# Optimization experiments

Measured on AMD Instinct MI355X. Metric: run time of the kernel, lower is better.

## Reference

```python
import jax, jax.numpy as jnp
import numpy as np

EPS = 1e-05
IN_FEATURES = 1024
OUT_FEATURES = 512
M = 65536


def setup_inputs() -> dict:
    key = jax.random.key(0)
    k_x, k_w, k_b = jax.random.split(key, 3)
    x = jax.random.normal(k_x, (M, IN_FEATURES), dtype=jnp.float32)
    # kaiming_uniform(a=sqrt(5)) on [out, in]: bound = sqrt(6/((1+a^2)*fan_in)) = 1/sqrt(fan_in)
    bound = 1.0 / np.sqrt(IN_FEATURES)
    weight = jax.random.uniform(k_w, (OUT_FEATURES, IN_FEATURES), dtype=jnp.float32,
                                minval=-bound, maxval=bound)
    bias = jax.random.uniform(k_b, (OUT_FEATURES,), dtype=jnp.float32,
                              minval=-bound, maxval=bound)
    gamma = jnp.ones((OUT_FEATURES,), dtype=jnp.float32)
    beta = jnp.zeros((OUT_FEATURES,), dtype=jnp.float32)
    scale = jnp.ones((1,), dtype=jnp.float32)
    return {"x": x, "weight": weight, "bias": bias,
            "gamma": gamma, "beta": beta, "scale": scale}


def reference(x, weight, bias, gamma, beta, scale):
    # GEMM + bias: [M, N]
    acc = jnp.einsum('mk,nk->mn', x, weight) + bias[None, :]
    # Row-wise normalization over N (as the fused kernel computes per row)
    mean = jnp.mean(acc, axis=1, keepdims=True)
    var = jnp.mean((acc - mean) ** 2, axis=1, keepdims=True)
    normalized = (acc - mean) / jnp.sqrt(var + EPS)
    scaled = (normalized * gamma[None, :] + beta[None, :]) * scale[0]
    # Row softmax over N
    return jax.nn.softmax(scaled, axis=1)
```

## Files before the change

### kernel.cpp

```cpp
#include <hip/hip_runtime.h>
#include <hip/hip_bf16.h>

constexpr int KD = 1024;
constexpr int ND = 512;
constexpr int NT = 32;
constexpr float EPSV = 1e-5f;

using f32x4  = __attribute__((ext_vector_type(4))) float;
using bf16x8 = __attribute__((ext_vector_type(8))) short;
using u16x8  = __attribute__((ext_vector_type(8))) unsigned short;

__device__ __forceinline__ unsigned short f2bf(float f) {
  unsigned int u = __builtin_bit_cast(unsigned int, f);
  return (unsigned short)((u + 0x7fffu + ((u >> 16) & 1u)) >> 16);
}

__device__ __forceinline__ u16x8 pack8(float4 a, float4 b) {
  u16x8 v;
  v[0] = f2bf(a.x); v[1] = f2bf(a.y); v[2] = f2bf(a.z); v[3] = f2bf(a.w);
  v[4] = f2bf(b.x); v[5] = f2bf(b.y); v[6] = f2bf(b.z); v[7] = f2bf(b.w);
  return v;
}

__device__ __forceinline__ unsigned short cvt1(float f) {
  __hip_bfloat16 h = __float2bfloat16(f);
  return __builtin_bit_cast(unsigned short, h);
}

#define SCHEDB()  __builtin_amdgcn_sched_barrier(0)

__global__ void wconvert_kernel(const float* __restrict__ w,
                                unsigned short* __restrict__ wb) {
  int uid = blockIdx.x * blockDim.x + threadIdx.x;
  int s   = uid >> 11;
  int nf  = (uid >> 6) & 31;
  int l   = uid & 63;
  int n   = nf * 16 + (l & 15);
  int k0  = s * 32 + (l >> 4) * 8;
  const float* src = w + n * KD + k0;
  float4 a = *reinterpret_cast<const float4*>(src);
  float4 b = *reinterpret_cast<const float4*>(src + 4);
  *reinterpret_cast<u16x8*>(wb + (size_t)uid * 8) = pack8(a, b);
}

__global__ __launch_bounds__(512, 4)
void fused_kernel(const float* __restrict__ x,
                  const unsigned short* __restrict__ wb,
                  const float* __restrict__ bias,
                  const float* __restrict__ gamma,
                  const float* __restrict__ beta,
                  const float* __restrict__ scalep,
                  float* __restrict__ out) {
  __shared__ unsigned short As[4][64 * 32];

  const int tid  = threadIdx.x;
  const int lane = tid & 63;
  const int wid  = tid >> 6;
  const int l15  = lane & 15;
  const int lg   = lane >> 4;

  const long bm  = (long)blockIdx.x * 64;

  f32x4 acc[4][4] = {};

  const int arow = tid >> 3;
  const int akq  = tid & 7;
  const float* asrc = x + (bm + arow) * KD + akq * 4;
  const int awb = arow * 64 + (((akq >> 1) ^ ((arow >> 1) & 3)) * 16)
                + ((akq & 1) * 8);

  const int swa = (lg ^ ((l15 >> 1) & 3)) * 16;
  int ard[4];
  #pragma unroll
  for (int mi = 0; mi < 4; ++mi) ard[mi] = (mi * 16 + l15) * 64 + swa;

  const unsigned short* bbase = wb + ((size_t)(wid * 4) * 64 + lane) * 8;

#define LOADA(t) (*reinterpret_cast<const float4*>(asrc + (t) * 32))

#define LOADB(t, r0, r1, r2, r3) do { \
    const unsigned short* bp_ = bbase + (size_t)(t) * 16384; \
    r0 = *reinterpret_cast<const bf16x8*>(bp_ + 0 * 512); \
    r1 = *reinterpret_cast<const bf16x8*>(bp_ + 1 * 512); \
    r2 = *reinterpret_cast<const bf16x8*>(bp_ + 2 * 512); \
    r3 = *reinterpret_cast<const bf16x8*>(bp_ + 3 * 512); } while (0)

#define WRITE_A(q_, bufi) do { \
    union { unsigned short s[4]; unsigned long long v; } c_; \
    c_.s[0] = cvt1(q_.x); c_.s[1] = cvt1(q_.y); \
    c_.s[2] = cvt1(q_.z); c_.s[3] = cvt1(q_.w); \
    *reinterpret_cast<unsigned long long*>((char*)As[bufi] + awb) = c_.v; } while (0)

#define COMPUTE(bufi, B0, B1, B2, B3) do { \
    const char* ab_ = (const char*)As[bufi]; \
    bf16x8 a0_ = *reinterpret_cast<const bf16x8*>(ab_ + ard[0]); \
    bf16x8 a1_ = *reinterpret_cast<const bf16x8*>(ab_ + ard[1]); \
    bf16x8 a2_ = *reinterpret_cast<const bf16x8*>(ab_ + ard[2]); \
    bf16x8 a3_ = *reinterpret_cast<const bf16x8*>(ab_ + ard[3]); \
    acc[0][0] = __builtin_amdgcn_mfma_f32_16x16x32_bf16(a0_, B0, acc[0][0], 0, 0, 0); \
    acc[0][1] = __builtin_amdgcn_mfma_f32_16x16x32_bf16(a0_, B1, acc[0][1], 0, 0, 0); \
    acc[0][2] = __builtin_amdgcn_mfma_f32_16x16x32_bf16(a0_, B2, acc[0][2], 0, 0, 0); \
    acc[0][3] = __builtin_amdgcn_mfma_f32_16x16x32_bf16(a0_, B3, acc[0][3], 0, 0, 0); \
    acc[1][0] = __builtin_amdgcn_mfma_f32_16x16x32_bf16(a1_, B0, acc[1][0], 0, 0, 0); \
    acc[1][1] = __builtin_amdgcn_mfma_f32_16x16x32_bf16(a1_, B1, acc[1][1], 0, 0, 0); \
    acc[1][2] = __builtin_amdgcn_mfma_f32_16x16x32_bf16(a1_, B2, acc[1][2], 0, 0, 0); \
    acc[1][3] = __builtin_amdgcn_mfma_f32_16x16x32_bf16(a1_, B3, acc[1][3], 0, 0, 0); \
    acc[2][0] = __builtin_amdgcn_mfma_f32_16x16x32_bf16(a2_, B0, acc[2][0], 0, 0, 0); \
    acc[2][1] = __builtin_amdgcn_mfma_f32_16x16x32_bf16(a2_, B1, acc[2][1], 0, 0, 0); \
    acc[2][2] = __builtin_amdgcn_mfma_f32_16x16x32_bf16(a2_, B2, acc[2][2], 0, 0, 0); \
    acc[2][3] = __builtin_amdgcn_mfma_f32_16x16x32_bf16(a2_, B3, acc[2][3], 0, 0, 0); \
    acc[3][0] = __builtin_amdgcn_mfma_f32_16x16x32_bf16(a3_, B0, acc[3][0], 0, 0, 0); \
    acc[3][1] = __builtin_amdgcn_mfma_f32_16x16x32_bf16(a3_, B1, acc[3][1], 0, 0, 0); \
    acc[3][2] = __builtin_amdgcn_mfma_f32_16x16x32_bf16(a3_, B2, acc[3][2], 0, 0, 0); \
    acc[3][3] = __builtin_amdgcn_mfma_f32_16x16x32_bf16(a3_, B3, acc[3][3], 0, 0, 0); \
    } while (0)

  float4 qaE, qaO;
  bf16x8 bc0, bc1, bc2, bc3, bn0, bn1, bn2, bn3;

  qaE = LOADA(0);
  qaO = LOADA(1);
  LOADB(0, bc0, bc1, bc2, bc3);
  WRITE_A(qaE, 0);
  WRITE_A(qaO, 1);
  __syncthreads();

  for (int t = 0; t < NT; t += 2) {
    const int b0 = t & 3;
    const int tp2 = (t + 2 < NT) ? t + 2 : NT - 1;
    const int tp3 = (t + 3 < NT) ? t + 3 : NT - 1;
    qaE = LOADA(tp2);
    qaO = LOADA(tp3);
    LOADB(t + 1 < NT ? t + 1 : NT - 1, bn0, bn1, bn2, bn3);
    SCHEDB();
    COMPUTE(b0, bc0, bc1, bc2, bc3);
    WRITE_A(qaE, (b0 + 2) & 3);
    LOADB(tp2, bc0, bc1, bc2, bc3);
    SCHEDB();
    COMPUTE((b0 + 1) & 3, bn0, bn1, bn2, bn3);
    WRITE_A(qaO, (b0 + 3) & 3);
    __syncthreads();
  }

  float* redS = (float*)As[0];
  float* redQ = redS + 576;
  float* rowA = redS + 1152;
  float* rowB = redS + 1216;

  const int col0 = wid * 64 + l15;
  const float sc = scalep[0];
  float bs4[4], gs4[4], bb4[4];
  #pragma unroll
  for (int ni = 0; ni < 4; ++ni) {
    bs4[ni] = bias[col0 + ni * 16];
    gs4[ni] = gamma[col0 + ni * 16] * sc;
    bb4[ni] = beta[col0 + ni * 16] * sc;
  }

  #pragma unroll
  for (int mi = 0; mi < 4; ++mi) {
    #pragma unroll
    for (int j = 0; j < 4; ++j) {
      float s = 0.f, q = 0.f;
      #pragma unroll
      for (int ni = 0; ni < 4; ++ni) {
        float v = acc[mi][ni][j] + bs4[ni];
        acc[mi][ni][j] = v;
        s += v;
        q = fmaf(v, v, q);
      }
      #pragma unroll
      for (int m = 1; m < 16; m <<= 1) {
        s += __shfl_xor(s, m, 64);
        q += __shfl_xor(q, m, 64);
      }
      if (l15 == 0) {
        int r = mi * 16 + lg * 4 + j;
        redS[r * 9 + wid] = s;
        redQ[r * 9 + wid] = q;
      }
    }
  }
  __syncthreads();
  if (tid < 64) {
    float s = 0.f, q = 0.f;
    #pragma unroll
    for (int k = 0; k < 8; ++k) { s += redS[tid * 9 + k]; q += redQ[tid * 9 + k]; }
    float mu = s * (1.f / ND);
    rowA[tid] = mu;
    rowB[tid] = rsqrtf(q * (1.f / ND) - mu * mu + EPSV);
  }
  __syncthreads();

  #pragma unroll
  for (int mi = 0; mi < 4; ++mi) {
    #pragma unroll
    for (int j = 0; j < 4; ++j) {
      int r = mi * 16 + lg * 4 + j;
      float mu = rowA[r], rs = rowB[r];
      float ps = 0.f;
      #pragma unroll
      for (int ni = 0; ni < 4; ++ni) {
        float v = (acc[mi][ni][j] - mu) * rs;
        v = fmaf(v, gs4[ni], bb4[ni]);
        float e = __expf(v);
        acc[mi][ni][j] = e;
        ps += e;
      }
      #pragma unroll
      for (int m = 1; m < 16; m <<= 1) ps += __shfl_xor(ps, m, 64);
      if (l15 == 0) redQ[r * 9 + wid] = ps;
    }
  }
  __syncthreads();
  if (tid < 64) {
    float s = 0.f;
    #pragma unroll
    for (int k = 0; k < 8; ++k) s += redQ[tid * 9 + k];
    rowB[tid] = 1.f / s;
  }
  __syncthreads();

  #pragma unroll
  for (int mi = 0; mi < 4; ++mi) {
    #pragma unroll
    for (int j = 0; j < 4; ++j) {
      int r = mi * 16 + lg * 4 + j;
      float rd = rowB[r];
      float* op = out + (bm + r) * ND + col0;
      #pragma unroll
      for (int ni = 0; ni < 4; ++ni)
        __builtin_nontemporal_store(acc[mi][ni][j] * rd, op + ni * 16);
    }
  }
#undef LOADA
#undef LOADB
#undef WRITE_A
#undef COMPUTE
}

__global__ void fused_fallback(const float* __restrict__ x,
                               const float* __restrict__ wf,
                               const float* __restrict__ bias,
                               const float* __restrict__ gamma,
                               const float* __restrict__ beta,
                               const float* __restrict__ scalep,
                               float* __restrict__ out) {
  long row = blockIdx.x;
  int t = threadIdx.x;
  float s = 0.f;
  const float* xr = x + row * KD;
  const float* wr_ = wf + (size_t)t * KD;
  for (int k = 0; k < KD; ++k) s += xr[k] * wr_[k];
  s += bias[t];
  __shared__ float buf[ND];
  buf[t] = s;
  __syncthreads();
  __shared__ float red[2];
  if (t == 0) {
    float sum = 0.f, sq = 0.f;
    for (int i = 0; i < ND; ++i) { sum += buf[i]; sq += buf[i] * buf[i]; }
    float mu = sum / ND;
    red[0] = mu;
    red[1] = rsqrtf(sq / ND - mu * mu + EPSV);
  }
  __syncthreads();
  float zv = (s - red[0]) * red[1] * gamma[t] * scalep[0] + beta[t] * scalep[0];
  buf[t] = zv;
  __syncthreads();
  __shared__ float red2[2];
  if (t == 0) {
    float mxv = -3.4e38f;
    for (int i = 0; i < ND; ++i) mxv = fmaxf(mxv, buf[i]);
    float den = 0.f;
    for (int i = 0; i < ND; ++i) den += __expf(buf[i] - mxv);
    red2[0] = mxv; red2[1] = 1.f / den;
  }
  __syncthreads();
  out[row * ND + t] = __expf(zv - red2[0]) * red2[1];
}

extern "C" void kernel_launch(void* const* d_in, const int* in_sizes, int n_in,
                              void* d_out, int out_size, void* d_ws, size_t ws_size,
                              hipStream_t stream) {
  const float* x     = (const float*)d_in[0];
  const float* w     = (const float*)d_in[1];
  const float* bias  = (const float*)d_in[2];
  const float* gamma = (const float*)d_in[3];
  const float* beta  = (const float*)d_in[4];
  const float* scale = (const float*)d_in[5];
  float* out = (float*)d_out;

  const int Mrows = in_sizes[0] / KD;
  const size_t wb_bytes = (size_t)ND * KD * sizeof(unsigned short);

  if (ws_size >= wb_bytes) {
    unsigned short* wbuf = (unsigned short*)d_ws;
    wconvert_kernel<<<(ND * KD / 8) / 256, 256, 0, stream>>>(w, wbuf);
    fused_kernel<<<Mrows / 64, 512, 0, stream>>>(x, wbuf, bias, gamma, beta,
                                                 scale, out);
  } else {
    fused_fallback<<<Mrows, ND, 0, stream>>>(x, w, bias, gamma, beta, scale, out);
  }
}
```

Before: 121.4 us.

## Give each wave a private double-buffered A tile to drop block barriers

Each of the eight waves now loads and converts the whole 64x32 fp32 A tile for every k-step into its own double-buffered LDS region. This removes the per-iteration __syncthreads from the main loop. The cost is that x is loaded and converted to bf16 eight times per block instead of once, which adds much more global/L2 traffic and VALU conversion work. LDS use per block also grows fourfold, which can lower how many blocks fit on a CU.

```diff
diff --git a/kernel.cpp b/kernel.cpp
--- a/kernel.cpp
+++ b/kernel.cpp
@@ -51,7 +51,7 @@
                   const float* __restrict__ beta,
                   const float* __restrict__ scalep,
                   float* __restrict__ out) {
-  __shared__ unsigned short As[4][64 * 32];
+  __shared__ unsigned short As[8][2][2048];
 
   const int tid  = threadIdx.x;
   const int lane = tid & 63;
@@ -63,86 +63,93 @@
 
   f32x4 acc[4][4] = {};
 
-  const int arow = tid >> 3;
-  const int akq  = tid & 7;
+  const int arow = lane >> 3;
+  const int akq  = lane & 7;
   const float* asrc = x + (bm + arow) * KD + akq * 4;
-  const int awb = arow * 64 + (((akq >> 1) ^ ((arow >> 1) & 3)) * 16)
-                + ((akq & 1) * 8);
-
-  const int swa = (lg ^ ((l15 >> 1) & 3)) * 16;
-  int ard[4];
-  #pragma unroll
-  for (int mi = 0; mi < 4; ++mi) ard[mi] = (mi * 16 + l15) * 64 + swa;
+  const int awb0 = arow * 64 + (((akq >> 1) ^ ((arow >> 1) & 3)) * 16)
+                 + ((akq & 1) * 8);
+
+  const int ardb = l15 * 64 + (lg ^ ((l15 >> 1) & 3)) * 16;
 
   const unsigned short* bbase = wb + ((size_t)(wid * 4) * 64 + lane) * 8;
 
-#define LOADA(t) (*reinterpret_cast<const float4*>(asrc + (t) * 32))
-
-#define LOADB(t, r0, r1, r2, r3) do { \
+  char* const buf0 = (char*)As[wid][0];
+  char* const buf1 = (char*)As[wid][1];
+
+#define ISSUE_A4(t, roff) do { \
+    qa0 = *reinterpret_cast<const float4*>(asrc + ((roff) + 0)  * KD + (t) * 32); \
+    qa1 = *reinterpret_cast<const float4*>(asrc + ((roff) + 8)  * KD + (t) * 32); \
+    qa2 = *reinterpret_cast<const float4*>(asrc + ((roff) + 16) * KD + (t) * 32); \
+    qa3 = *reinterpret_cast<const float4*>(asrc + ((roff) + 24) * KD + (t) * 32); } while (0)
+
+#define WRITE_A4(bufp, boff) do { \
+    union { unsigned short s[4]; unsigned long long v; } c0_, c1_, c2_, c3_; \
+    c0_.s[0] = cvt1(qa0.x); c0_.s[1] = cvt1(qa0.y); \
+    c0_.s[2] = cvt1(qa0.z); c0_.s[3] = cvt1(qa0.w); \
+    c1_.s[0] = cvt1(qa1.x); c1_.s[1] = cvt1(qa1.y); \
+    c1_.s[2] = cvt1(qa1.z); c1_.s[3] = cvt1(qa1.w); \
+    c2_.s[0] = cvt1(qa2.x); c2_.s[1] = cvt1(qa2.y); \
+    c2_.s[2] = cvt1(qa2.z); c2_.s[3] = cvt1(qa2.w); \
+    c3_.s[0] = cvt1(qa3.x); c3_.s[1] = cvt1(qa3.y); \
+    c3_.s[2] = cvt1(qa3.z); c3_.s[3] = cvt1(qa3.w); \
+    *reinterpret_cast<unsigned long long*>((bufp) + awb0 + (boff) + 0 * 512) = c0_.v; \
+    *reinterpret_cast<unsigned long long*>((bufp) + awb0 + (boff) + 1 * 512) = c1_.v; \
+    *reinterpret_cast<unsigned long long*>((bufp) + awb0 + (boff) + 2 * 512) = c2_.v; \
+    *reinterpret_cast<unsigned long long*>((bufp) + awb0 + (boff) + 3 * 512) = c3_.v; } while (0)
+
+#define ISSUE_B(t) do { \
     const unsigned short* bp_ = bbase + (size_t)(t) * 16384; \
-    r0 = *reinterpret_cast<const bf16x8*>(bp_ + 0 * 512); \
-    r1 = *reinterpret_cast<const bf16x8*>(bp_ + 1 * 512); \
-    r2 = *reinterpret_cast<const bf16x8*>(bp_ + 2 * 512); \
-    r3 = *reinterpret_cast<const bf16x8*>(bp_ + 3 * 512); } while (0)
-
-#define WRITE_A(q_, bufi) do { \
-    union { unsigned short s[4]; unsigned long long v; } c_; \
-    c_.s[0] = cvt1(q_.x); c_.s[1] = cvt1(q_.y); \
-    c_.s[2] = cvt1(q_.z); c_.s[3] = cvt1(q_.w); \
-    *reinterpret_cast<unsigned long long*>((char*)As[bufi] + awb) = c_.v; } while (0)
-
-#define COMPUTE(bufi, B0, B1, B2, B3) do { \
-    const char* ab_ = (const char*)As[bufi]; \
-    bf16x8 a0_ = *reinterpret_cast<const bf16x8*>(ab_ + ard[0]); \
-    bf16x8 a1_ = *reinterpret_cast<const bf16x8*>(ab_ + ard[1]); \
-    bf16x8 a2_ = *reinterpret_cast<const bf16x8*>(ab_ + ard[2]); \
-    bf16x8 a3_ = *reinterpret_cast<const bf16x8*>(ab_ + ard[3]); \
-    acc[0][0] = __builtin_amdgcn_mfma_f32_16x16x32_bf16(a0_, B0, acc[0][0], 0, 0, 0); \
-    acc[0][1] = __builtin_amdgcn_mfma_f32_16x16x32_bf16(a0_, B1, acc[0][1], 0, 0, 0); \
-    acc[0][2] = __builtin_amdgcn_mfma_f32_16x16x32_bf16(a0_, B2, acc[0][2], 0, 0, 0); \
-    acc[0][3] = __builtin_amdgcn_mfma_f32_16x16x32_bf16(a0_, B3, acc[0][3], 0, 0, 0); \
-    acc[1][0] = __builtin_amdgcn_mfma_f32_16x16x32_bf16(a1_, B0, acc[1][0], 0, 0, 0); \
-    acc[1][1] = __builtin_amdgcn_mfma_f32_16x16x32_bf16(a1_, B1, acc[1][1], 0, 0, 0); \
-    acc[1][2] = __builtin_amdgcn_mfma_f32_16x16x32_bf16(a1_, B2, acc[1][2], 0, 0, 0); \
-    acc[1][3] = __builtin_amdgcn_mfma_f32_16x16x32_bf16(a1_, B3, acc[1][3], 0, 0, 0); \
-    acc[2][0] = __builtin_amdgcn_mfma_f32_16x16x32_bf16(a2_, B0, acc[2][0], 0, 0, 0); \
-    acc[2][1] = __builtin_amdgcn_mfma_f32_16x16x32_bf16(a2_, B1, acc[2][1], 0, 0, 0); \
-    acc[2][2] = __builtin_amdgcn_mfma_f32_16x16x32_bf16(a2_, B2, acc[2][2], 0, 0, 0); \
-    acc[2][3] = __builtin_amdgcn_mfma_f32_16x16x32_bf16(a2_, B3, acc[2][3], 0, 0, 0); \
-    acc[3][0] = __builtin_amdgcn_mfma_f32_16x16x32_bf16(a3_, B0, acc[3][0], 0, 0, 0); \
-    acc[3][1] = __builtin_amdgcn_mfma_f32_16x16x32_bf16(a3_, B1, acc[3][1], 0, 0, 0); \
-    acc[3][2] = __builtin_amdgcn_mfma_f32_16x16x32_bf16(a3_, B2, acc[3][2], 0, 0, 0); \
-    acc[3][3] = __builtin_amdgcn_mfma_f32_16x16x32_bf16(a3_, B3, acc[3][3], 0, 0, 0); \
+    bc0 = *reinterpret_cast<const bf16x8*>(bp_ + 0 * 512); \
+    bc1 = *reinterpret_cast<const bf16x8*>(bp_ + 1 * 512); \
+    bc2 = *reinterpret_cast<const bf16x8*>(bp_ + 2 * 512); \
+    bc3 = *reinterpret_cast<const bf16x8*>(bp_ + 3 * 512); } while (0)
+
+#define COMPUTE(bufp) do { \
+    bf16x8 a0_ = *reinterpret_cast<const bf16x8*>((bufp) + ardb + 0 * 1024); \
+    bf16x8 a1_ = *reinterpret_cast<const bf16x8*>((bufp) + ardb + 1 * 1024); \
+    bf16x8 a2_ = *reinterpret_cast<const bf16x8*>((bufp) + ardb + 2 * 1024); \
+    bf16x8 a3_ = *reinterpret_cast<const bf16x8*>((bufp) + ardb + 3 * 1024); \
+    acc[0][0] = __builtin_amdgcn_mfma_f32_16x16x32_bf16(a0_, bc0, acc[0][0], 0, 0, 0); \
+    acc[0][1] = __builtin_amdgcn_mfma_f32_16x16x32_bf16(a0_, bc1, acc[0][1], 0, 0, 0); \
+    acc[0][2] = __builtin_amdgcn_mfma_f32_16x16x32_bf16(a0_, bc2, acc[0][2], 0, 0, 0); \
+    acc[0][3] = __builtin_amdgcn_mfma_f32_16x16x32_bf16(a0_, bc3, acc[0][3], 0, 0, 0); \
+    acc[1][0] = __builtin_amdgcn_mfma_f32_16x16x32_bf16(a1_, bc0, acc[1][0], 0, 0, 0); \
+    acc[1][1] = __builtin_amdgcn_mfma_f32_16x16x32_bf16(a1_, bc1, acc[1][1], 0, 0, 0); \
+    acc[1][2] = __builtin_amdgcn_mfma_f32_16x16x32_bf16(a1_, bc2, acc[1][2], 0, 0, 0); \
+    acc[1][3] = __builtin_amdgcn_mfma_f32_16x16x32_bf16(a1_, bc3, acc[1][3], 0, 0, 0); \
+    acc[2][0] = __builtin_amdgcn_mfma_f32_16x16x32_bf16(a2_, bc0, acc[2][0], 0, 0, 0); \
+    acc[2][1] = __builtin_amdgcn_mfma_f32_16x16x32_bf16(a2_, bc1, acc[2][1], 0, 0, 0); \
+    acc[2][2] = __builtin_amdgcn_mfma_f32_16x16x32_bf16(a2_, bc2, acc[2][2], 0, 0, 0); \
+    acc[2][3] = __builtin_amdgcn_mfma_f32_16x16x32_bf16(a2_, bc3, acc[2][3], 0, 0, 0); \
+    acc[3][0] = __builtin_amdgcn_mfma_f32_16x16x32_bf16(a3_, bc0, acc[3][0], 0, 0, 0); \
+    acc[3][1] = __builtin_amdgcn_mfma_f32_16x16x32_bf16(a3_, bc1, acc[3][1], 0, 0, 0); \
+    acc[3][2] = __builtin_amdgcn_mfma_f32_16x16x32_bf16(a3_, bc2, acc[3][2], 0, 0, 0); \
+    acc[3][3] = __builtin_amdgcn_mfma_f32_16x16x32_bf16(a3_, bc3, acc[3][3], 0, 0, 0); \
     } while (0)
 
-  float4 qaE, qaO;
-  bf16x8 bc0, bc1, bc2, bc3, bn0, bn1, bn2, bn3;
-
-  qaE = LOADA(0);
-  qaO = LOADA(1);
-  LOADB(0, bc0, bc1, bc2, bc3);
-  WRITE_A(qaE, 0);
-  WRITE_A(qaO, 1);
-  __syncthreads();
-
-  for (int t = 0; t < NT; t += 2) {
-    const int b0 = t & 3;
-    const int tp2 = (t + 2 < NT) ? t + 2 : NT - 1;
-    const int tp3 = (t + 3 < NT) ? t + 3 : NT - 1;
-    qaE = LOADA(tp2);
-    qaO = LOADA(tp3);
-    LOADB(t + 1 < NT ? t + 1 : NT - 1, bn0, bn1, bn2, bn3);
+  float4 qa0, qa1, qa2, qa3;
+  bf16x8 bc0, bc1, bc2, bc3;
+
+  ISSUE_A4(0, 0);  WRITE_A4(buf0, 0);
+  ISSUE_A4(0, 32); WRITE_A4(buf0, 2048);
+
+  #pragma unroll 2
+  for (int t = 0; t < NT; ++t) {
+    char* const curp = (t & 1) ? buf1 : buf0;
+    char* const nxtp = (t & 1) ? buf0 : buf1;
+    const int tp1 = (t + 1 < NT) ? t + 1 : NT - 1;
+    ISSUE_B(t);
+    ISSUE_A4(tp1, 0);
     SCHEDB();
-    COMPUTE(b0, bc0, bc1, bc2, bc3);
-    WRITE_A(qaE, (b0 + 2) & 3);
-    LOADB(tp2, bc0, bc1, bc2, bc3);
-    SCHEDB();
-    COMPUTE((b0 + 1) & 3, bn0, bn1, bn2, bn3);
-    WRITE_A(qaO, (b0 + 3) & 3);
-    __syncthreads();
-  }
-
-  float* redS = (float*)As[0];
+    COMPUTE(curp);
+    WRITE_A4(nxtp, 0);
+    ISSUE_A4(tp1, 32);
+    WRITE_A4(nxtp, 2048);
+  }
+
+  __syncthreads();
+
+  float* redS = (float*)&As[0][0][0];
   float* redQ = redS + 576;
   float* rowA = redS + 1152;
   float* rowB = redS + 1216;
@@ -233,9 +240,9 @@
         __builtin_nontemporal_store(acc[mi][ni][j] * rd, op + ni * 16);
     }
   }
-#undef LOADA
-#undef LOADB
-#undef WRITE_A
+#undef ISSUE_A4
+#undef WRITE_A4
+#undef ISSUE_B
 #undef COMPUTE
 }
 
```

Measured after the change: 214.8 us. +77.0%, slower.

## Stage A tile in two big halves in LDS, drop per-K-step barriers

Applied to the files above, without the earlier changes.

Replaces the four-slot rotating A ring buffer, which needed a barrier every two K steps, with one 64KB LDS tile holding half the K range. Each half is loaded, converted to bf16 and stored with an XOR swizzle in a single phase, then 16 unrolled MFMA steps run without barriers. This removes the frequent __syncthreads and gives wider loads, but global loads of A no longer overlap with compute. The 64KB LDS per block will also cut occupancy below the four blocks per CU that the launch bounds request.

```diff
diff --git a/kernel.cpp b/kernel.cpp
--- a/kernel.cpp
+++ b/kernel.cpp
@@ -3,7 +3,6 @@
 
 constexpr int KD = 1024;
 constexpr int ND = 512;
-constexpr int NT = 32;
 constexpr float EPSV = 1e-5f;
 
 using f32x4  = __attribute__((ext_vector_type(4))) float;
@@ -20,11 +19,6 @@
   v[0] = f2bf(a.x); v[1] = f2bf(a.y); v[2] = f2bf(a.z); v[3] = f2bf(a.w);
   v[4] = f2bf(b.x); v[5] = f2bf(b.y); v[6] = f2bf(b.z); v[7] = f2bf(b.w);
   return v;
-}
-
-__device__ __forceinline__ unsigned short cvt1(float f) {
-  __hip_bfloat16 h = __float2bfloat16(f);
-  return __builtin_bit_cast(unsigned short, h);
 }
 
 #define SCHEDB()  __builtin_amdgcn_sched_barrier(0)
@@ -51,32 +45,42 @@
                   const float* __restrict__ beta,
                   const float* __restrict__ scalep,
                   float* __restrict__ out) {
-  __shared__ unsigned short As[4][64 * 32];
+  __shared__ unsigned short Ares[64 * 512];
 
   const int tid  = threadIdx.x;
   const int lane = tid & 63;
   const int wid  = tid >> 6;
   const int l15  = lane & 15;
   const int lg   = lane >> 4;
+  const int rq   = l15 & 7;
 
   const long bm  = (long)blockIdx.x * 64;
 
   f32x4 acc[4][4] = {};
 
-  const int arow = tid >> 3;
-  const int akq  = tid & 7;
-  const float* asrc = x + (bm + arow) * KD + akq * 4;
-  const int awb = arow * 64 + (((akq >> 1) ^ ((arow >> 1) & 3)) * 16)
-                + ((akq & 1) * 8);
-
-  const int swa = (lg ^ ((l15 >> 1) & 3)) * 16;
-  int ard[4];
-  #pragma unroll
-  for (int mi = 0; mi < 4; ++mi) ard[mi] = (mi * 16 + l15) * 64 + swa;
+  const int r  = tid >> 3;
+  const int c  = tid & 7;
+  const int rs = r & 7;
+  const float* xsrc = x + (bm + r) * KD + c * 64;
+  char* const lbase = (char*)Ares + r * 1024 + c * 128;
+
+  const char* const ab = (const char*)Ares + l15 * 1024;
 
   const unsigned short* bbase = wb + ((size_t)(wid * 4) * 64 + lane) * 8;
 
-#define LOADA(t) (*reinterpret_cast<const float4*>(asrc + (t) * 32))
+#define STAGE(h) do { \
+    const float* sp_ = xsrc + (h) * 512; \
+    _Pragma("unroll") \
+    for (int b = 0; b < 4; ++b) { \
+      float4 f0_ = *reinterpret_cast<const float4*>(sp_ + b * 16 + 0); \
+      float4 f1_ = *reinterpret_cast<const float4*>(sp_ + b * 16 + 4); \
+      float4 f2_ = *reinterpret_cast<const float4*>(sp_ + b * 16 + 8); \
+      float4 f3_ = *reinterpret_cast<const float4*>(sp_ + b * 16 + 12); \
+      u16x8 c0_ = pack8(f0_, f1_); \
+      u16x8 c1_ = pack8(f2_, f3_); \
+      *reinterpret_cast<u16x8*>(lbase + (((2 * b + 0) ^ rs) << 4)) = c0_; \
+      *reinterpret_cast<u16x8*>(lbase + (((2 * b + 1) ^ rs) << 4)) = c1_; \
+    } } while (0)
 
 #define LOADB(t, r0, r1, r2, r3) do { \
     const unsigned short* bp_ = bbase + (size_t)(t) * 16384; \
@@ -85,18 +89,12 @@
     r2 = *reinterpret_cast<const bf16x8*>(bp_ + 2 * 512); \
     r3 = *reinterpret_cast<const bf16x8*>(bp_ + 3 * 512); } while (0)
 
-#define WRITE_A(q_, bufi) do { \
-    union { unsigned short s[4]; unsigned long long v; } c_; \
-    c_.s[0] = cvt1(q_.x); c_.s[1] = cvt1(q_.y); \
-    c_.s[2] = cvt1(q_.z); c_.s[3] = cvt1(q_.w); \
-    *reinterpret_cast<unsigned long long*>((char*)As[bufi] + awb) = c_.v; } while (0)
-
-#define COMPUTE(bufi, B0, B1, B2, B3) do { \
-    const char* ab_ = (const char*)As[bufi]; \
-    bf16x8 a0_ = *reinterpret_cast<const bf16x8*>(ab_ + ard[0]); \
-    bf16x8 a1_ = *reinterpret_cast<const bf16x8*>(ab_ + ard[1]); \
-    bf16x8 a2_ = *reinterpret_cast<const bf16x8*>(ab_ + ard[2]); \
-    bf16x8 a3_ = *reinterpret_cast<const bf16x8*>(ab_ + ard[3]); \
+#define COMPUTE(ks, B0, B1, B2, B3) do { \
+    const int qo_ = ((((ks) * 4 + lg) ^ rq) << 4); \
+    bf16x8 a0_ = *reinterpret_cast<const bf16x8*>(ab + 0 * 16384 + qo_); \
+    bf16x8 a1_ = *reinterpret_cast<const bf16x8*>(ab + 1 * 16384 + qo_); \
+    bf16x8 a2_ = *reinterpret_cast<const bf16x8*>(ab + 2 * 16384 + qo_); \
+    bf16x8 a3_ = *reinterpret_cast<const bf16x8*>(ab + 3 * 16384 + qo_); \
     acc[0][0] = __builtin_amdgcn_mfma_f32_16x16x32_bf16(a0_, B0, acc[0][0], 0, 0, 0); \
     acc[0][1] = __builtin_amdgcn_mfma_f32_16x16x32_bf16(a0_, B1, acc[0][1], 0, 0, 0); \
     acc[0][2] = __builtin_amdgcn_mfma_f32_16x16x32_bf16(a0_, B2, acc[0][2], 0, 0, 0); \
@@ -115,34 +113,36 @@
     acc[3][3] = __builtin_amdgcn_mfma_f32_16x16x32_bf16(a3_, B3, acc[3][3], 0, 0, 0); \
     } while (0)
 
-  float4 qaE, qaO;
   bf16x8 bc0, bc1, bc2, bc3, bn0, bn1, bn2, bn3;
 
-  qaE = LOADA(0);
-  qaO = LOADA(1);
+  STAGE(0);
+  __syncthreads();
   LOADB(0, bc0, bc1, bc2, bc3);
-  WRITE_A(qaE, 0);
-  WRITE_A(qaO, 1);
-  __syncthreads();
-
-  for (int t = 0; t < NT; t += 2) {
-    const int b0 = t & 3;
-    const int tp2 = (t + 2 < NT) ? t + 2 : NT - 1;
-    const int tp3 = (t + 3 < NT) ? t + 3 : NT - 1;
-    qaE = LOADA(tp2);
-    qaO = LOADA(tp3);
-    LOADB(t + 1 < NT ? t + 1 : NT - 1, bn0, bn1, bn2, bn3);
+  #pragma unroll
+  for (int ks = 0; ks < 16; ks += 2) {
+    LOADB(ks + 1, bn0, bn1, bn2, bn3);
     SCHEDB();
-    COMPUTE(b0, bc0, bc1, bc2, bc3);
-    WRITE_A(qaE, (b0 + 2) & 3);
-    LOADB(tp2, bc0, bc1, bc2, bc3);
+    COMPUTE(ks, bc0, bc1, bc2, bc3);
+    LOADB(ks + 2, bc0, bc1, bc2, bc3);
     SCHEDB();
-    COMPUTE((b0 + 1) & 3, bn0, bn1, bn2, bn3);
-    WRITE_A(qaO, (b0 + 3) & 3);
-    __syncthreads();
-  }
-
-  float* redS = (float*)As[0];
+    COMPUTE(ks + 1, bn0, bn1, bn2, bn3);
+  }
+
+  __syncthreads();
+  STAGE(1);
+  __syncthreads();
+  #pragma unroll
+  for (int ks = 0; ks < 16; ks += 2) {
+    LOADB(17 + ks, bn0, bn1, bn2, bn3);
+    SCHEDB();
+    COMPUTE(ks, bc0, bc1, bc2, bc3);
+    LOADB(18 + ks < 32 ? 18 + ks : 31, bc0, bc1, bc2, bc3);
+    SCHEDB();
+    COMPUTE(ks + 1, bn0, bn1, bn2, bn3);
+  }
+  __syncthreads();
+
+  float* redS = (float*)Ares;
   float* redQ = redS + 576;
   float* rowA = redS + 1152;
   float* rowB = redS + 1216;
@@ -175,9 +175,9 @@
         q += __shfl_xor(q, m, 64);
       }
       if (l15 == 0) {
-        int r = mi * 16 + lg * 4 + j;
-        redS[r * 9 + wid] = s;
-        redQ[r * 9 + wid] = q;
+        int rr = mi * 16 + lg * 4 + j;
+        redS[rr * 9 + wid] = s;
+        redQ[rr * 9 + wid] = q;
       }
     }
   }
@@ -196,12 +196,12 @@
   for (int mi = 0; mi < 4; ++mi) {
     #pragma unroll
     for (int j = 0; j < 4; ++j) {
-      int r = mi * 16 + lg * 4 + j;
-      float mu = rowA[r], rs = rowB[r];
+      int rr = mi * 16 + lg * 4 + j;
+      float mu = rowA[rr], rstd = rowB[rr];
       float ps = 0.f;
       #pragma unroll
       for (int ni = 0; ni < 4; ++ni) {
-        float v = (acc[mi][ni][j] - mu) * rs;
+        float v = (acc[mi][ni][j] - mu) * rstd;
         v = fmaf(v, gs4[ni], bb4[ni]);
         float e = __expf(v);
         acc[mi][ni][j] = e;
@@ -209,7 +209,7 @@
       }
       #pragma unroll
       for (int m = 1; m < 16; m <<= 1) ps += __shfl_xor(ps, m, 64);
-      if (l15 == 0) redQ[r * 9 + wid] = ps;
+      if (l15 == 0) redQ[rr * 9 + wid] = ps;
     }
   }
   __syncthreads();
@@ -225,17 +225,16 @@
   for (int mi = 0; mi < 4; ++mi) {
     #pragma unroll
     for (int j = 0; j < 4; ++j) {
-      int r = mi * 16 + lg * 4 + j;
-      float rd = rowB[r];
-      float* op = out + (bm + r) * ND + col0;
+      int rr = mi * 16 + lg * 4 + j;
+      float rd = rowB[rr];
+      float* op = out + (bm + rr) * ND + col0;
       #pragma unroll
       for (int ni = 0; ni < 4; ++ni)
         __builtin_nontemporal_store(acc[mi][ni][j] * rd, op + ni * 16);
     }
   }
-#undef LOADA
+#undef STAGE
 #undef LOADB
-#undef WRITE_A
 #undef COMPUTE
 }
 
```

Result: slower. 156.1 us (+28.6%).
